# Kernel tuning notes

Hardware: AMD Instinct MI355X
Metric: run time of the kernel (lower is better)

The kernel has to match this reference:

```python
import jax, jax.numpy as jnp
import numpy as np

B, S, D, E, H, K = 4, 2048, 1024, 8, 4096, 2


def setup_inputs() -> dict:
    key = jax.random.key(0)
    ks = jax.random.split(key, 6)
    scale_in = 0.02  # keep logits/activations in a sane range
    return {
        "x": jax.random.normal(ks[0], (B, S, D), jnp.float32),
        "gate_w": jax.random.normal(ks[1], (D, E), jnp.float32) * scale_in,
        "noise_weight": jnp.zeros((E,), jnp.float32),  # torch init: zeros
        "noise": jax.random.normal(ks[2], (B, S, E), jnp.float32),
        "w1": jax.random.normal(ks[3], (E, D, H), jnp.float32) * scale_in,
        "b1": jnp.zeros((E, H), jnp.float32),
        "w2": jax.random.normal(ks[4], (E, D, H), jnp.float32) * scale_in,
        "b2": jnp.zeros((E, H), jnp.float32),
        "wp": jax.random.normal(ks[5], (E, H, D), jnp.float32) * scale_in,
        "bp": jnp.zeros((E, D), jnp.float32),
    }


def _moe(x, gate_w, noise_weight, noise, w1, b1, w2, b2, wp, bp):
    b, s, d = x.shape
    # --- noisy top-k gate ---
    logits = jnp.einsum("bsd,de->bse", x, gate_w)          # [B,S,E]
    logits_noisy = logits + noise * noise_weight            # noisy_std = 1.0
    top_v, top_i = jax.lax.top_k(logits_noisy, K)           # [B,S,K]
    # softmax over sparse logits (-inf elsewhere) == softmax over the top-k values
    probs_k = jax.nn.softmax(top_v, axis=-1)                # [B,S,K]
    onehot = jax.nn.one_hot(top_i, E, dtype=x.dtype)        # [B,S,K,E]
    gated = jnp.einsum("bsk,bske->bse", probs_k, onehot)    # [B,S,E]

    # --- dispatch / expert SwiGLU / weighted combine ---
    xf = x.reshape(b * s, d)                                # [T,D]
    gf = gated.reshape(b * s, E).T                          # [E,T]

    def body(acc, p):
        w1e, b1e, w2e, b2e, wpe, bpe, ge = p
        h = (xf @ w1e + b1e) * jax.nn.silu(xf @ w2e + b2e)  # [T,H] SwiGLU
        out = h @ wpe + bpe                                 # [T,D]
        return acc + ge[:, None] * out, None

    acc, _ = jax.lax.scan(body, jnp.zeros_like(xf), (w1, b1, w2, b2, wp, bp, gf))
    return acc.reshape(b, s, d)


def reference(x, gate_w, noise_weight, noise, w1, b1, w2, b2, wp, bp):
    return _moe(x, gate_w, noise_weight, noise, w1, b1, w2, b2, wp, bp)
```

## Files before the change

kernel.cpp:

```cpp
#include <hip/hip_runtime.h>


#define T_TOK 8192
#define DDIM 1024
#define EEXP 8
#define HDIM 4096
#define RMAX 18432

typedef short short8 __attribute__((ext_vector_type(8)));
typedef float f32x4 __attribute__((ext_vector_type(4)));
typedef unsigned short ushort4v __attribute__((ext_vector_type(4)));
typedef unsigned int u32;

__device__ __forceinline__ unsigned short f2bf(float f) {
  unsigned u = __builtin_bit_cast(unsigned, f);
  return (unsigned short)((u + 0x7FFFu + ((u >> 16) & 1u)) >> 16);
}
__device__ __forceinline__ float bf2f(unsigned short b) {
  unsigned u = ((unsigned)b) << 16;
  return __builtin_bit_cast(float, u);
}
__device__ __forceinline__ void gl_lds16(const void* g, void* l) {
  __builtin_amdgcn_global_load_lds((const u32 __attribute__((address_space(1)))*)g,
                                   (u32 __attribute__((address_space(3)))*)l, 16, 0, 0);
}
#define BAR() asm volatile("s_barrier" ::: "memory")
__device__ __forceinline__ void vwait_c(int n) {
  if (n == 8) asm volatile("s_waitcnt vmcnt(8)" ::: "memory");
  else if (n == 4) asm volatile("s_waitcnt vmcnt(4)" ::: "memory");
  else if (n == 0) asm volatile("s_waitcnt vmcnt(0)" ::: "memory");
}
#define MFMA_BF16 __builtin_amdgcn_mfma_f32_16x16x32_bf16

__global__ void k_convert_w(const float* __restrict__ src, unsigned short* __restrict__ dst,
                            int N, int K) {
  __shared__ float lbuf[32][130];
  int e = blockIdx.z, ct = blockIdx.x, kt = blockIdx.y;
  int tid = threadIdx.x;
  const float* s = src + (size_t)e * K * N + (size_t)(kt * 32) * N + ct * 128;
#pragma unroll
  for (int q = 0; q < 4; q++) {
    int idx = q * 256 + tid;
    int row = idx >> 5, c4 = (idx & 31) * 4;
    float4 v = *(const float4*)(s + (size_t)row * N + c4);
    lbuf[row][c4 + 0] = v.x; lbuf[row][c4 + 1] = v.y;
    lbuf[row][c4 + 2] = v.z; lbuf[row][c4 + 3] = v.w;
  }
  __syncthreads();
  char* dt = (char*)dst + ((size_t)(e * (N / 128) + ct) * (K / 32) + kt) * 8192;
#pragma unroll
  for (int q = 0; q < 2; q++) {
    int idx = q * 256 + tid;
    int n = idx >> 2, kc = idx & 3;
    short8 o;
#pragma unroll
    for (int j = 0; j < 8; j++) o[j] = (short)f2bf(lbuf[kc * 8 + j][n]);
    *(short8*)(dt + ((n * 64 + kc * 16) ^ ((n & 3) << 4))) = o;
  }
}

__global__ void k_init(int* __restrict__ rowtok, int* __restrict__ counts, int* __restrict__ cursor) {
  int i = blockIdx.x * 256 + threadIdx.x;
  if (i < RMAX) rowtok[i] = 0;
  if (i < EEXP) { counts[i] = 0; cursor[i] = 0; }
}

__launch_bounds__(256)
__global__ void k_gate(const float* __restrict__ x, const float* __restrict__ gw,
                       const float* __restrict__ nwt, const float* __restrict__ noi,
                       int* __restrict__ tki, float* __restrict__ tkp,
                       int* __restrict__ counts, unsigned short* __restrict__ xb) {
  __shared__ float gwT[8][1024];
  int tid = threadIdx.x;
#pragma unroll
  for (int q = 0; q < 32; q++) {
    int flat = q * 256 + tid;
    gwT[flat & 7][flat >> 3] = gw[flat];
  }
  __syncthreads();
  int wave = tid >> 6, l = tid & 63;
  int t = blockIdx.x * 4 + wave;
  float acc[8] = {0.f, 0.f, 0.f, 0.f, 0.f, 0.f, 0.f, 0.f};
  const float4* xr = (const float4*)(x + (size_t)t * DDIM);
#pragma unroll
  for (int i = 0; i < 4; i++) {
    float4 xv = xr[l + i * 64];
    int d0 = (l + i * 64) * 4;
    ushort4v o;
    o.x = f2bf(xv.x); o.y = f2bf(xv.y); o.z = f2bf(xv.z); o.w = f2bf(xv.w);
    *(ushort4v*)(xb + (size_t)t * DDIM + d0) = o;
#pragma unroll
    for (int e = 0; e < 8; e++) {
      float4 gv = *(const float4*)&gwT[e][d0];
      acc[e] += xv.x * gv.x + xv.y * gv.y + xv.z * gv.z + xv.w * gv.w;
    }
  }
#pragma unroll
  for (int s = 1; s < 64; s <<= 1) {
#pragma unroll
    for (int e = 0; e < 8; e++) acc[e] += __shfl_xor(acc[e], s, 64);
  }
  if (l == 0) {
    float nl[8];
#pragma unroll
    for (int e = 0; e < 8; e++) nl[e] = acc[e] + noi[t * 8 + e] * nwt[e];
    int i0 = 0; float v0 = nl[0];
#pragma unroll
    for (int e = 1; e < 8; e++) if (nl[e] > v0) { v0 = nl[e]; i0 = e; }
    int i1 = -1; float v1 = -3.4e38f;
#pragma unroll
    for (int e = 0; e < 8; e++) if (e != i0 && nl[e] > v1) { v1 = nl[e]; i1 = e; }
    float ex = __expf(v1 - v0);
    float p0 = 1.f / (1.f + ex);
    float p1 = ex * p0;
    tki[2 * t] = i0; tki[2 * t + 1] = i1;
    tkp[2 * t] = p0; tkp[2 * t + 1] = p1;
    atomicAdd(&counts[i0], 1);
    atomicAdd(&counts[i1], 1);
  }
}

__global__ void k_prefix(const int* __restrict__ counts, int* __restrict__ basep) {
  if (threadIdx.x == 0) {
    int b = 0;
    for (int e = 0; e < EEXP; e++) { basep[e] = b; b += (counts[e] + 255) & ~255; }
  }
}

__global__ void k_scatter(const int* __restrict__ tki, const int* __restrict__ basep,
                          int* __restrict__ cursor, int* __restrict__ rowtok,
                          int* __restrict__ t2r) {
  int t = blockIdx.x * 256 + threadIdx.x;
  if (t >= T_TOK) return;
#pragma unroll
  for (int k = 0; k < 2; k++) {
    int e = tki[2 * t + k];
    int pos = atomicAdd(&cursor[e], 1);
    int row = basep[e] + pos;
    rowtok[row] = t;
    t2r[2 * t + k] = row;
  }
}

__launch_bounds__(512, 2)
__global__ void k_gemm1(const unsigned short* __restrict__ xb,
                        const unsigned short* __restrict__ w1s, const unsigned short* __restrict__ w2s,
                        const float* __restrict__ b1g, const float* __restrict__ b2g,
                        const int* __restrict__ counts, const int* __restrict__ basep,
                        const int* __restrict__ rowtok,
                        unsigned short* __restrict__ hout) {
  int e = blockIdx.y >> 6;
  int rt = blockIdx.y & 63;
  int cnt = counts[e];
  if (rt >= ((cnt + 255) >> 8)) return;
  int ct = blockIdx.x;
  int row0 = basep[e] + rt * 256;
  int col0 = ct * 128;

  __shared__ char smem[131072];
  __shared__ int s_tok[256];
  __shared__ float s_b1[128], s_b2[128];

  int tid = threadIdx.x;
  if (tid < 256) s_tok[tid] = rowtok[row0 + tid];
  if (tid < 128) {
    s_b1[tid] = b1g[e * HDIM + col0 + tid];
    s_b2[tid] = b2g[e * HDIM + col0 + tid];
  }
  __syncthreads();

  int wave = tid >> 6, l = tid & 63;
  int wm = wave >> 2, wn = wave & 3;
  int g = l >> 4, ln = l & 15;

  int c0 = tid, c1 = 512 + tid;
  int r0s = c0 >> 2, k0s = c0 & 3, r1s = c1 >> 2, k1s = c1 & 3;
  size_t a_src0 = (size_t)s_tok[r0s] * 2048 + (size_t)((k0s ^ (r0s & 3)) * 16);
  size_t a_src1 = (size_t)s_tok[r1s] * 2048 + (size_t)((k1s ^ (r1s & 3)) * 16);
  int a_dst0 = c0 * 16, a_dst1 = c1 * 16;

  int a_rd[8];
#pragma unroll
  for (int m = 0; m < 8; m++) {
    int r = wm * 128 + m * 16 + ln;
    a_rd[m] = r * 64 + ((g * 16) ^ ((r & 3) << 4));
  }
  int b_rd[2];
#pragma unroll
  for (int n = 0; n < 2; n++) {
    int r = wn * 32 + n * 16 + ln;
    b_rd[n] = r * 64 + ((g * 16) ^ ((r & 3) << 4));
  }

  f32x4 zero = {0.f, 0.f, 0.f, 0.f};
  f32x4 acc_a[8][2], acc_b[8][2];
#pragma unroll
  for (int m = 0; m < 8; m++)
#pragma unroll
    for (int n = 0; n < 2; n++) { acc_a[m][n] = zero; acc_b[m][n] = zero; }

  const char* xbb = (const char*)xb;
  const char* w1t = (const char*)w1s + (size_t)(e * 32 + ct) * 32 * 8192;
  const char* w2t = (const char*)w2s + (size_t)(e * 32 + ct) * 32 * 8192;

#define G1_PRE(s) { int nb = (s) & 3;                                            \
    gl_lds16(xbb + a_src0 + (size_t)(s) * 64, smem + nb * 16384 + a_dst0);       \
    gl_lds16(xbb + a_src1 + (size_t)(s) * 64, smem + nb * 16384 + a_dst1);       \
    gl_lds16(w1t + (size_t)(s) * 8192 + tid * 16, smem + 65536 + nb * 8192 + tid * 16); \
    gl_lds16(w2t + (size_t)(s) * 8192 + tid * 16, smem + 98304 + nb * 8192 + tid * 16); }

  G1_PRE(0) G1_PRE(1) G1_PRE(2)
  vwait_c(8); BAR();

#define G1_SLOT(s, ISSUE, VMN) {                                                 \
    int bs = (s) & 3;                                                            \
    char* Ab = smem + bs * 16384;                                                \
    char* B1b = smem + 65536 + bs * 8192;                                        \
    char* B2b = smem + 98304 + bs * 8192;                                        \
    short8 af[4], b1f[2], b2f[2];                                                \
    _Pragma("unroll") for (int m = 0; m < 4; m++) af[m] = *(const short8*)(Ab + a_rd[m]); \
    b1f[0] = *(const short8*)(B1b + b_rd[0]); b1f[1] = *(const short8*)(B1b + b_rd[1]); \
    b2f[0] = *(const short8*)(B2b + b_rd[0]); b2f[1] = *(const short8*)(B2b + b_rd[1]); \
    if (ISSUE) { int ns = (s) + 3, nb = ns & 3;                                  \
      gl_lds16(xbb + a_src0 + (size_t)ns * 64, smem + nb * 16384 + a_dst0);      \
      gl_lds16(xbb + a_src1 + (size_t)ns * 64, smem + nb * 16384 + a_dst1); }    \
    BAR();                                                                       \
    __builtin_amdgcn_s_setprio(1);                                               \
    _Pragma("unroll") for (int m = 0; m < 4; m++) {                              \
      acc_a[m][0] = MFMA_BF16(af[m], b1f[0], acc_a[m][0], 0, 0, 0);              \
      acc_a[m][1] = MFMA_BF16(af[m], b1f[1], acc_a[m][1], 0, 0, 0);              \
      acc_b[m][0] = MFMA_BF16(af[m], b2f[0], acc_b[m][0], 0, 0, 0);              \
      acc_b[m][1] = MFMA_BF16(af[m], b2f[1], acc_b[m][1], 0, 0, 0); }            \
    __builtin_amdgcn_s_setprio(0);                                               \
    BAR();                                                                       \
    _Pragma("unroll") for (int m = 0; m < 4; m++) af[m] = *(const short8*)(Ab + a_rd[4 + m]); \
    if (ISSUE) { int ns = (s) + 3, nb = ns & 3;                                  \
      gl_lds16(w1t + (size_t)ns * 8192 + tid * 16, smem + 65536 + nb * 8192 + tid * 16); \
      gl_lds16(w2t + (size_t)ns * 8192 + tid * 16, smem + 98304 + nb * 8192 + tid * 16); } \
    BAR();                                                                       \
    __builtin_amdgcn_s_setprio(1);                                               \
    _Pragma("unroll") for (int m = 0; m < 4; m++) {                              \
      acc_a[4 + m][0] = MFMA_BF16(af[m], b1f[0], acc_a[4 + m][0], 0, 0, 0);      \
      acc_a[4 + m][1] = MFMA_BF16(af[m], b1f[1], acc_a[4 + m][1], 0, 0, 0);      \
      acc_b[4 + m][0] = MFMA_BF16(af[m], b2f[0], acc_b[4 + m][0], 0, 0, 0);      \
      acc_b[4 + m][1] = MFMA_BF16(af[m], b2f[1], acc_b[4 + m][1], 0, 0, 0); }    \
    __builtin_amdgcn_s_setprio(0);                                               \
    vwait_c(VMN); BAR(); }

  for (int s = 0; s < 29; ++s) { G1_SLOT(s, 1, 8) }
  G1_SLOT(29, 0, 4)
  G1_SLOT(30, 0, 0)
  G1_SLOT(31, 0, -1)

  __syncthreads();
  unsigned short* ht = (unsigned short*)smem;
#pragma unroll
  for (int m = 0; m < 8; m++)
#pragma unroll
    for (int n = 0; n < 2; n++)
#pragma unroll
      for (int r = 0; r < 4; r++) {
        int row = wm * 128 + m * 16 + g * 4 + r;
        int col = wn * 32 + n * 16 + ln;
        float a = acc_a[m][n][r] + s_b1[col];
        float b = acc_b[m][n][r] + s_b2[col];
        float hv = a * (b / (1.f + __expf(-b)));
        ht[row * 128 + col] = f2bf(hv);
      }
  __syncthreads();
#pragma unroll
  for (int q = 0; q < 8; q++) {
    int idx = q * 512 + tid;
    int row = idx >> 4, cc = (idx & 15) * 8;
    short8 v = *(const short8*)(smem + idx * 16);
    *(short8*)(hout + (size_t)(row0 + row) * HDIM + col0 + cc) = v;
  }
}

__launch_bounds__(512, 2)
__global__ void k_gemm2(const unsigned short* __restrict__ hin,
                        const unsigned short* __restrict__ wps, const float* __restrict__ bpg,
                        const int* __restrict__ counts, const int* __restrict__ basep,
                        unsigned short* __restrict__ yout) {
  int e = blockIdx.y >> 6;
  int rt = blockIdx.y & 63;
  int cnt = counts[e];
  if (rt >= ((cnt + 255) >> 8)) return;
  int ct = blockIdx.x;
  int row0 = basep[e] + rt * 256;
  int col0 = ct * 256;

  __shared__ char smem[131072];
  __shared__ float s_bp[256];
  int tid = threadIdx.x;
  if (tid < 256) s_bp[tid] = bpg[e * DDIM + col0 + tid];
  __syncthreads();

  int wave = tid >> 6, l = tid & 63;
  int wm = wave >> 2, wn = wave & 3;
  int g = l >> 4, ln = l & 15;

  int c0 = tid, c1 = 512 + tid;
  int r0s = c0 >> 2, k0s = c0 & 3, r1s = c1 >> 2, k1s = c1 & 3;
  size_t a_src0 = (size_t)(row0 + r0s) * 8192 + (size_t)((k0s ^ (r0s & 3)) * 16);
  size_t a_src1 = (size_t)(row0 + r1s) * 8192 + (size_t)((k1s ^ (r1s & 3)) * 16);
  int a_dst0 = c0 * 16, a_dst1 = c1 * 16;
  const char* b_src0 = (const char*)wps + (size_t)(e * 8 + ct * 2 + 0) * 128 * 8192 + (size_t)(c0 & 511) * 16;
  const char* b_src1 = (const char*)wps + (size_t)(e * 8 + ct * 2 + 1) * 128 * 8192 + (size_t)(c1 & 511) * 16;

  int a_rd[8];
#pragma unroll
  for (int m = 0; m < 8; m++) {
    int r = wm * 128 + m * 16 + ln;
    a_rd[m] = r * 64 + ((g * 16) ^ ((r & 3) << 4));
  }
  int b_rd[4];
#pragma unroll
  for (int n = 0; n < 4; n++) {
    int ncol = wn * 64 + n * 16 + ln;
    int sub = ncol >> 7, r = ncol & 127;
    b_rd[n] = sub * 8192 + r * 64 + ((g * 16) ^ ((r & 3) << 4));
  }

  f32x4 zero = {0.f, 0.f, 0.f, 0.f};
  f32x4 acc[8][4];
#pragma unroll
  for (int m = 0; m < 8; m++)
#pragma unroll
    for (int n = 0; n < 4; n++) acc[m][n] = zero;

  const char* hb = (const char*)hin;

#define G2_PRE(s) { int nb = (s) & 3;                                            \
    gl_lds16(hb + a_src0 + (size_t)(s) * 64, smem + nb * 16384 + a_dst0);        \
    gl_lds16(hb + a_src1 + (size_t)(s) * 64, smem + nb * 16384 + a_dst1);        \
    gl_lds16(b_src0 + (size_t)(s) * 8192, smem + 65536 + nb * 16384 + a_dst0);   \
    gl_lds16(b_src1 + (size_t)(s) * 8192, smem + 65536 + nb * 16384 + a_dst1); }

  G2_PRE(0) G2_PRE(1) G2_PRE(2)
  vwait_c(8); BAR();

#define G2_SLOT(s, ISSUE, VMN) {                                                 \
    int bs = (s) & 3;                                                            \
    char* Ab = smem + bs * 16384;                                                \
    char* Bb = smem + 65536 + bs * 16384;                                        \
    short8 af[4], bf[4];                                                         \
    _Pragma("unroll") for (int m = 0; m < 4; m++) af[m] = *(const short8*)(Ab + a_rd[m]); \
    _Pragma("unroll") for (int n = 0; n < 4; n++) bf[n] = *(const short8*)(Bb + b_rd[n]); \
    if (ISSUE) { int ns = (s) + 3, nb = ns & 3;                                  \
      gl_lds16(hb + a_src0 + (size_t)ns * 64, smem + nb * 16384 + a_dst0);       \
      gl_lds16(hb + a_src1 + (size_t)ns * 64, smem + nb * 16384 + a_dst1); }     \
    BAR();                                                                       \
    __builtin_amdgcn_s_setprio(1);                                               \
    _Pragma("unroll") for (int m = 0; m < 4; m++)                                \
      _Pragma("unroll") for (int n = 0; n < 4; n++)                              \
        acc[m][n] = MFMA_BF16(af[m], bf[n], acc[m][n], 0, 0, 0);                 \
    __builtin_amdgcn_s_setprio(0);                                               \
    BAR();                                                                       \
    _Pragma("unroll") for (int m = 0; m < 4; m++) af[m] = *(const short8*)(Ab + a_rd[4 + m]); \
    if (ISSUE) { int ns = (s) + 3, nb = ns & 3;                                  \
      gl_lds16(b_src0 + (size_t)ns * 8192, smem + 65536 + nb * 16384 + a_dst0);  \
      gl_lds16(b_src1 + (size_t)ns * 8192, smem + 65536 + nb * 16384 + a_dst1); }\
    BAR();                                                                       \
    __builtin_amdgcn_s_setprio(1);                                               \
    _Pragma("unroll") for (int m = 0; m < 4; m++)                                \
      _Pragma("unroll") for (int n = 0; n < 4; n++)                              \
        acc[4 + m][n] = MFMA_BF16(af[m], bf[n], acc[4 + m][n], 0, 0, 0);         \
    __builtin_amdgcn_s_setprio(0);                                               \
    vwait_c(VMN); BAR(); }

  for (int s = 0; s < 125; ++s) { G2_SLOT(s, 1, 8) }
  G2_SLOT(125, 0, 4)
  G2_SLOT(126, 0, 0)
  G2_SLOT(127, 0, -1)

  __syncthreads();
  unsigned short* ht = (unsigned short*)smem;
#pragma unroll
  for (int m = 0; m < 8; m++)
#pragma unroll
    for (int n = 0; n < 4; n++)
#pragma unroll
      for (int r = 0; r < 4; r++) {
        int row = wm * 128 + m * 16 + g * 4 + r;
        int col = wn * 64 + n * 16 + ln;
        ht[row * 256 + col] = f2bf(acc[m][n][r] + s_bp[col]);
      }
  __syncthreads();
#pragma unroll
  for (int q = 0; q < 16; q++) {
    int idx = q * 512 + tid;
    int row = idx >> 5, cc = (idx & 31) * 8;
    short8 v = *(const short8*)(smem + idx * 16);
    *(short8*)(yout + (size_t)(row0 + row) * DDIM + col0 + cc) = v;
  }
}

__global__ void k_combine(const unsigned short* __restrict__ yv,
                          const int* __restrict__ t2r, const float* __restrict__ tkp,
                          float* __restrict__ outp) {
  int gid = blockIdx.x * 256 + threadIdx.x;
  int t = gid >> 8;
  int c4 = (gid & 255) << 2;
  int r0 = t2r[2 * t], r1 = t2r[2 * t + 1];
  float p0 = tkp[2 * t], p1 = tkp[2 * t + 1];
  ushort4v u0 = *(const ushort4v*)(yv + (size_t)r0 * DDIM + c4);
  ushort4v u1 = *(const ushort4v*)(yv + (size_t)r1 * DDIM + c4);
  float4 o;
  o.x = p0 * bf2f(u0.x) + p1 * bf2f(u1.x);
  o.y = p0 * bf2f(u0.y) + p1 * bf2f(u1.y);
  o.z = p0 * bf2f(u0.z) + p1 * bf2f(u1.z);
  o.w = p0 * bf2f(u0.w) + p1 * bf2f(u1.w);
  *(float4*)(outp + (size_t)t * DDIM + c4) = o;
}

extern "C" void kernel_launch(void* const* d_in, const int* in_sizes, int n_in,
                              void* d_out, int out_size, void* d_ws, size_t ws_size,
                              hipStream_t stream) {
  const float* x   = (const float*)d_in[0];
  const float* gw  = (const float*)d_in[1];
  const float* nwt = (const float*)d_in[2];
  const float* noi = (const float*)d_in[3];
  const float* w1  = (const float*)d_in[4];
  const float* b1  = (const float*)d_in[5];
  const float* w2  = (const float*)d_in[6];
  const float* b2  = (const float*)d_in[7];
  const float* wp  = (const float*)d_in[8];
  const float* bp  = (const float*)d_in[9];
  float* outp = (float*)d_out;
  char* ws = (char*)d_ws;

  constexpr size_t SZ_W = (size_t)EEXP * DDIM * HDIM * 2;
  constexpr size_t OFF_XB  = 0;
  constexpr size_t OFF_W1S = OFF_XB + (size_t)T_TOK * DDIM * 2;
  constexpr size_t OFF_W2S = OFF_W1S + SZ_W;
  constexpr size_t OFF_WPS = OFF_W2S + SZ_W;
  constexpr size_t OFF_H   = OFF_WPS + SZ_W;
  constexpr size_t OFF_Y   = OFF_H + (size_t)RMAX * HDIM * 2;
  constexpr size_t OFF_RT  = OFF_Y + (size_t)RMAX * DDIM * 2;
  constexpr size_t OFF_TKI = OFF_RT + (size_t)RMAX * 4;
  constexpr size_t OFF_TKP = OFF_TKI + (size_t)T_TOK * 2 * 4;
  constexpr size_t OFF_T2R = OFF_TKP + (size_t)T_TOK * 2 * 4;
  constexpr size_t OFF_CNT = OFF_T2R + (size_t)T_TOK * 2 * 4;
  constexpr size_t OFF_BAS = OFF_CNT + 256;
  constexpr size_t OFF_CUR = OFF_BAS + 256;

  unsigned short* xb  = (unsigned short*)(ws + OFF_XB);
  unsigned short* w1s = (unsigned short*)(ws + OFF_W1S);
  unsigned short* w2s = (unsigned short*)(ws + OFF_W2S);
  unsigned short* wps = (unsigned short*)(ws + OFF_WPS);
  unsigned short* h   = (unsigned short*)(ws + OFF_H);
  unsigned short* y   = (unsigned short*)(ws + OFF_Y);
  int*   rowtok = (int*)(ws + OFF_RT);
  int*   tki    = (int*)(ws + OFF_TKI);
  float* tkp    = (float*)(ws + OFF_TKP);
  int*   t2r    = (int*)(ws + OFF_T2R);
  int*   counts = (int*)(ws + OFF_CNT);
  int*   basep  = (int*)(ws + OFF_BAS);
  int*   cursor = (int*)(ws + OFF_CUR);

  dim3 blk(256);
  k_init<<<dim3((RMAX + 255) / 256), blk, 0, stream>>>(rowtok, counts, cursor);
  k_gate<<<dim3(T_TOK / 4), blk, 0, stream>>>(x, gw, nwt, noi, tki, tkp, counts, xb);
  k_convert_w<<<dim3(HDIM / 128, DDIM / 32, EEXP), blk, 0, stream>>>(w1, w1s, HDIM, DDIM);
  k_convert_w<<<dim3(HDIM / 128, DDIM / 32, EEXP), blk, 0, stream>>>(w2, w2s, HDIM, DDIM);
  k_convert_w<<<dim3(DDIM / 128, HDIM / 32, EEXP), blk, 0, stream>>>(wp, wps, DDIM, HDIM);
  k_prefix<<<dim3(1), dim3(64), 0, stream>>>(counts, basep);
  k_scatter<<<dim3(T_TOK / 256), blk, 0, stream>>>(tki, basep, cursor, rowtok, t2r);
  k_gemm1<<<dim3(HDIM / 128, EEXP * 64), dim3(512), 0, stream>>>(xb, w1s, w2s, b1, b2, counts, basep, rowtok, h);
  k_gemm2<<<dim3(DDIM / 256, EEXP * 64), dim3(512), 0, stream>>>(h, wps, bp, counts, basep, y);
  k_combine<<<dim3(T_TOK), blk, 0, stream>>>(y, t2r, tkp, outp);
  (void)in_sizes; (void)n_in; (void)out_size; (void)ws_size;
}
```

Measured before the change: 1.041 ms.

## Use stronger LDS swizzle for GEMM tiles and merge weight conversion kernels

Replaces the 4-way XOR swizzle of the bf16 LDS tiles with a wider swizzle that mixes row bits into the 16-byte column index. Weight conversion, global-to-LDS load mappings (via an inverse map) and the MFMA fragment reads in both GEMMs are updated to match. The aim is to remove LDS bank conflicts on the fragment reads. The three weight-conversion launches are also merged into one kernel with a flattened grid, which saves launch overhead. The gemm2 B-tile loads are simplified to contiguous per-thread copies, and the global access pattern for A loads becomes less sequential.

```diff
diff --git a/kernel.cpp b/kernel.cpp
--- a/kernel.cpp
+++ b/kernel.cpp
@@ -32,10 +32,27 @@
 }
 #define MFMA_BF16 __builtin_amdgcn_mfma_f32_16x16x32_bf16
 
-__global__ void k_convert_w(const float* __restrict__ src, unsigned short* __restrict__ dst,
-                            int N, int K) {
+__device__ __forceinline__ int swz(int r, int kc16) {
+  return (r * 64) ^ kc16 ^ (((r >> 1) & 7) << 4);
+}
+
+__global__ void k_convert_all(const float* __restrict__ w1, const float* __restrict__ w2,
+                              const float* __restrict__ wp,
+                              unsigned short* __restrict__ w1s, unsigned short* __restrict__ w2s,
+                              unsigned short* __restrict__ wps) {
   __shared__ float lbuf[32][130];
-  int e = blockIdx.z, ct = blockIdx.x, kt = blockIdx.y;
+  int bid = blockIdx.x;
+  int seg = bid >> 13;
+  int t = bid & 8191;
+  const float* src; unsigned short* dst; int N, K, ct, kt, e;
+  e = t >> 10;
+  if (seg < 2) {
+    src = (seg == 0) ? w1 : w2; dst = (seg == 0) ? w1s : w2s;
+    N = HDIM; K = DDIM; ct = (t >> 5) & 31; kt = t & 31;
+  } else {
+    src = wp; dst = wps;
+    N = DDIM; K = HDIM; ct = (t >> 7) & 7; kt = t & 127;
+  }
   int tid = threadIdx.x;
   const float* s = src + (size_t)e * K * N + (size_t)(kt * 32) * N + ct * 128;
 #pragma unroll
@@ -55,7 +72,7 @@
     short8 o;
 #pragma unroll
     for (int j = 0; j < 8; j++) o[j] = (short)f2bf(lbuf[kc * 8 + j][n]);
-    *(short8*)(dt + ((n * 64 + kc * 16) ^ ((n & 3) << 4))) = o;
+    *(short8*)(dt + swz(n, kc * 16)) = o;
   }
 }
 
@@ -141,6 +158,10 @@
     t2r[2 * t + k] = row;
   }
 }
+
+#define INV_MAP(c, r, kc) { int _h = (c) >> 3;                                   \
+    r = 2 * _h + ((((c) >> 2) ^ (_h >> 2)) & 1);                                 \
+    kc = ((c) & 3) ^ (_h & 3); }
 
 __launch_bounds__(512, 2)
 __global__ void k_gemm1(const unsigned short* __restrict__ xb,
@@ -174,22 +195,23 @@
   int g = l >> 4, ln = l & 15;
 
   int c0 = tid, c1 = 512 + tid;
-  int r0s = c0 >> 2, k0s = c0 & 3, r1s = c1 >> 2, k1s = c1 & 3;
-  size_t a_src0 = (size_t)s_tok[r0s] * 2048 + (size_t)((k0s ^ (r0s & 3)) * 16);
-  size_t a_src1 = (size_t)s_tok[r1s] * 2048 + (size_t)((k1s ^ (r1s & 3)) * 16);
+  int r0, kc0, r1, kc1;
+  INV_MAP(c0, r0, kc0) INV_MAP(c1, r1, kc1)
+  size_t a_src0 = (size_t)s_tok[r0] * 2048 + (size_t)(kc0 * 16);
+  size_t a_src1 = (size_t)s_tok[r1] * 2048 + (size_t)(kc1 * 16);
   int a_dst0 = c0 * 16, a_dst1 = c1 * 16;
 
   int a_rd[8];
 #pragma unroll
   for (int m = 0; m < 8; m++) {
     int r = wm * 128 + m * 16 + ln;
-    a_rd[m] = r * 64 + ((g * 16) ^ ((r & 3) << 4));
+    a_rd[m] = swz(r, g * 16);
   }
   int b_rd[2];
 #pragma unroll
   for (int n = 0; n < 2; n++) {
     int r = wn * 32 + n * 16 + ln;
-    b_rd[n] = r * 64 + ((g * 16) ^ ((r & 3) << 4));
+    b_rd[n] = swz(r, g * 16);
   }
 
   f32x4 zero = {0.f, 0.f, 0.f, 0.f};
@@ -301,25 +323,26 @@
   int g = l >> 4, ln = l & 15;
 
   int c0 = tid, c1 = 512 + tid;
-  int r0s = c0 >> 2, k0s = c0 & 3, r1s = c1 >> 2, k1s = c1 & 3;
-  size_t a_src0 = (size_t)(row0 + r0s) * 8192 + (size_t)((k0s ^ (r0s & 3)) * 16);
-  size_t a_src1 = (size_t)(row0 + r1s) * 8192 + (size_t)((k1s ^ (r1s & 3)) * 16);
+  int r0, kc0, r1, kc1;
+  INV_MAP(c0, r0, kc0) INV_MAP(c1, r1, kc1)
+  size_t a_src0 = (size_t)(row0 + r0) * 8192 + (size_t)(kc0 * 16);
+  size_t a_src1 = (size_t)(row0 + r1) * 8192 + (size_t)(kc1 * 16);
   int a_dst0 = c0 * 16, a_dst1 = c1 * 16;
-  const char* b_src0 = (const char*)wps + (size_t)(e * 8 + ct * 2 + 0) * 128 * 8192 + (size_t)(c0 & 511) * 16;
-  const char* b_src1 = (const char*)wps + (size_t)(e * 8 + ct * 2 + 1) * 128 * 8192 + (size_t)(c1 & 511) * 16;
+  const char* b_src0 = (const char*)wps + (size_t)(e * 8 + ct * 2 + 0) * 128 * 8192 + (size_t)tid * 16;
+  const char* b_src1 = (const char*)wps + (size_t)(e * 8 + ct * 2 + 1) * 128 * 8192 + (size_t)tid * 16;
 
   int a_rd[8];
 #pragma unroll
   for (int m = 0; m < 8; m++) {
     int r = wm * 128 + m * 16 + ln;
-    a_rd[m] = r * 64 + ((g * 16) ^ ((r & 3) << 4));
+    a_rd[m] = swz(r, g * 16);
   }
   int b_rd[4];
 #pragma unroll
   for (int n = 0; n < 4; n++) {
     int ncol = wn * 64 + n * 16 + ln;
     int sub = ncol >> 7, r = ncol & 127;
-    b_rd[n] = sub * 8192 + r * 64 + ((g * 16) ^ ((r & 3) << 4));
+    b_rd[n] = sub * 8192 + swz(r, g * 16);
   }
 
   f32x4 zero = {0.f, 0.f, 0.f, 0.f};
@@ -334,8 +357,8 @@
 #define G2_PRE(s) { int nb = (s) & 3;                                            \
     gl_lds16(hb + a_src0 + (size_t)(s) * 64, smem + nb * 16384 + a_dst0);        \
     gl_lds16(hb + a_src1 + (size_t)(s) * 64, smem + nb * 16384 + a_dst1);        \
-    gl_lds16(b_src0 + (size_t)(s) * 8192, smem + 65536 + nb * 16384 + a_dst0);   \
-    gl_lds16(b_src1 + (size_t)(s) * 8192, smem + 65536 + nb * 16384 + a_dst1); }
+    gl_lds16(b_src0 + (size_t)(s) * 8192, smem + 65536 + nb * 16384 + tid * 16); \
+    gl_lds16(b_src1 + (size_t)(s) * 8192, smem + 65536 + nb * 16384 + 8192 + tid * 16); }
 
   G2_PRE(0) G2_PRE(1) G2_PRE(2)
   vwait_c(8); BAR();
@@ -359,8 +382,8 @@
     BAR();                                                                       \
     _Pragma("unroll") for (int m = 0; m < 4; m++) af[m] = *(const short8*)(Ab + a_rd[4 + m]); \
     if (ISSUE) { int ns = (s) + 3, nb = ns & 3;                                  \
-      gl_lds16(b_src0 + (size_t)ns * 8192, smem + 65536 + nb * 16384 + a_dst0);  \
-      gl_lds16(b_src1 + (size_t)ns * 8192, smem + 65536 + nb * 16384 + a_dst1); }\
+      gl_lds16(b_src0 + (size_t)ns * 8192, smem + 65536 + nb * 16384 + tid * 16);\
+      gl_lds16(b_src1 + (size_t)ns * 8192, smem + 65536 + nb * 16384 + 8192 + tid * 16); }\
     BAR();                                                                       \
     __builtin_amdgcn_s_setprio(1);                                               \
     _Pragma("unroll") for (int m = 0; m < 4; m++)                                \
@@ -462,9 +485,7 @@
   dim3 blk(256);
   k_init<<<dim3((RMAX + 255) / 256), blk, 0, stream>>>(rowtok, counts, cursor);
   k_gate<<<dim3(T_TOK / 4), blk, 0, stream>>>(x, gw, nwt, noi, tki, tkp, counts, xb);
-  k_convert_w<<<dim3(HDIM / 128, DDIM / 32, EEXP), blk, 0, stream>>>(w1, w1s, HDIM, DDIM);
-  k_convert_w<<<dim3(HDIM / 128, DDIM / 32, EEXP), blk, 0, stream>>>(w2, w2s, HDIM, DDIM);
-  k_convert_w<<<dim3(DDIM / 128, HDIM / 32, EEXP), blk, 0, stream>>>(wp, wps, DDIM, HDIM);
+  k_convert_all<<<dim3(24576), blk, 0, stream>>>(w1, w2, wp, w1s, w2s, wps);
   k_prefix<<<dim3(1), dim3(64), 0, stream>>>(counts, basep);
   k_scatter<<<dim3(T_TOK / 256), blk, 0, stream>>>(tki, basep, cursor, rowtok, t2r);
   k_gemm1<<<dim3(HDIM / 128, EEXP * 64), dim3(512), 0, stream>>>(xb, w1s, w2s, b1, b2, counts, basep, rowtok, h);
```

Measured after the change: 1.029 ms. No clear change (-1.1%).
